# Kernel tuning notes

Hardware: AMD Instinct MI355X
Metric: run time of the kernel (lower is better)

## Reference

```python
import jax, jax.numpy as jnp
import numpy as np

KHS = 3        # kernel_half_size
SIGMA = 1.6    # sigma / dx
DX = 1.0
C = 20.0       # accumulate() hard-codes c = 20


def _gauss_kernel():
    size = 2 * KHS + 1
    g = np.arange(size, dtype=np.float32) - (size - 1) / 2.0
    g = np.exp(-(g / SIGMA) ** 2 / 2.0) / (SIGMA * np.sqrt(2.0 * np.pi))
    k = g[:, None, None] * g[None, :, None] * g[None, None, :]
    k = k / k.sum()
    return jnp.asarray(k[None, None], dtype=jnp.float32)  # [1,1,7,7,7]


def _smooth(x, kernel):
    # depthwise (single-channel) 3d gaussian conv, 'same' padding, zero bias
    return jax.lax.conv_general_dilated(
        x, kernel, window_strides=(1, 1, 1),
        padding=[(KHS, KHS)] * 3,
        dimension_numbers=("NCDHW", "OIDHW", "NCDHW"))


def _fdiff(f, axis):
    # forward difference, replicate last difference to keep size (torchJacobian3 style)
    d = jnp.diff(f, axis=axis)
    last = jax.lax.slice_in_dim(d, d.shape[axis] - 1, d.shape[axis], axis=axis)
    return jnp.concatenate([d, last], axis=axis)


def _curl(v):
    # v: [B,3,D,H,W]; per-channel fields are [B,D,H,W]; z->axis1, y->axis2, x->axis3
    u, vv, w = v[:, 0], v[:, 1], v[:, 2]
    cu = _fdiff(w, 2) - _fdiff(vv, 1)   # dw/dy - dv/dz
    cv = _fdiff(u, 1) - _fdiff(w, 3)    # du/dz - dw/dx
    cw = _fdiff(vv, 3) - _fdiff(u, 2)   # dv/dx - du/dy
    return jnp.stack([cu, cv, cw], axis=1)


def _integrate(t, v):
    # trapezoidal transmittance-weighted integral along depth (dim 2)
    front = (1.0 - t[:, :, 0]) * v[:, :, 0]
    trap = jnp.sum((t[:, :, :-1] - t[:, :, 1:]) * (v[:, :, :-1] + v[:, :, 1:]) * 0.5, axis=2)
    return front + trap


def setup_inputs() -> dict:
    key = jax.random.key(0)
    k1, k2 = jax.random.split(key)
    d = jax.random.uniform(k1, (4, 1, 128, 128, 128), dtype=jnp.float32)
    v = jax.random.normal(k2, (4, 3, 128, 128, 128), dtype=jnp.float32)
    return {"d": d, "v": v}


def reference(d, v):
    kern = _gauss_kernel()
    ds = _smooth(d, kern)
    vort = _curl(v) / DX
    vn = jnp.sqrt(jnp.sum(vort ** 2, axis=1, keepdims=True))  # [B,1,D,H,W]
    vn = _smooth(vn, kern)
    # single default view dir 'zp' -> identity rotation
    df = jnp.flip(ds, axis=2)
    vf = jnp.flip(vn, axis=2)
    x = jnp.cumsum(df * DX, axis=2)
    t = (x * C + 1.0) * jnp.exp(-C * x)
    iv = _integrate(t, vf)              # [B,1,H,W]
    return jnp.clip(iv, 0.0, 1.0)
```

## Files before the change

kernel.cpp:

```cpp
#include <hip/hip_runtime.h>
#include <math.h>

#define NB 4
#define DD 128
#define HH 128
#define WW 128
#define VOX (DD*HH*WW)
#define NVOX (NB*VOX)

struct GaussW { float w[7]; };
struct CurlIn { float4 wc, wyn, vc, vzn, uc, uzn, uyn; float wxp, vxp; };

__device__ __forceinline__ float4 f4zero() { float4 z; z.x = z.y = z.z = z.w = 0.f; return z; }

__device__ __forceinline__ CurlIn curl4_load(const float* __restrict__ u,
                                             const float* __restrict__ vv,
                                             const float* __restrict__ w,
                                             int z, int y, int x0) {
    int xq = x0 >> 2;
    size_t s = ((size_t)z << 14) | ((size_t)y << 7) | (size_t)x0;
    int dy = (y < 127) ? 128 : -128;
    int dz = (z < 127) ? 16384 : -16384;
    int dxp = (xq < 31) ? 4 : 0;
    CurlIn ci;
    ci.wc  = *(const float4*)(w  + s);
    ci.wyn = *(const float4*)(w  + s + dy);
    ci.vc  = *(const float4*)(vv + s);
    ci.vzn = *(const float4*)(vv + s + dz);
    ci.uc  = *(const float4*)(u  + s);
    ci.uzn = *(const float4*)(u  + s + dz);
    ci.uyn = *(const float4*)(u  + s + dy);
    ci.wxp = w [s + 3 + dxp];
    ci.vxp = vv[s + 3 + dxp];
    return ci;
}

__device__ __forceinline__ float4 curl4_math(const CurlIn& ci, int z, int y, int x0) {
    float sy = (y < 127) ? 1.f : -1.f;
    float sz = (z < 127) ? 1.f : -1.f;
    float wca[4] = {ci.wc.x, ci.wc.y, ci.wc.z, ci.wc.w};
    float vca[4] = {ci.vc.x, ci.vc.y, ci.vc.z, ci.vc.w};
    float wya[4] = {ci.wyn.x, ci.wyn.y, ci.wyn.z, ci.wyn.w};
    float vza[4] = {ci.vzn.x, ci.vzn.y, ci.vzn.z, ci.vzn.w};
    float uca[4] = {ci.uc.x, ci.uc.y, ci.uc.z, ci.uc.w};
    float uza[4] = {ci.uzn.x, ci.uzn.y, ci.uzn.z, ci.uzn.w};
    float uya[4] = {ci.uyn.x, ci.uyn.y, ci.uyn.z, ci.uyn.w};
    float wsh[4] = {ci.wc.y, ci.wc.z, ci.wc.w, ci.wxp};
    float vsh[4] = {ci.vc.y, ci.vc.z, ci.vc.w, ci.vxp};

    float4 o;
    float* oa = &o.x;
#pragma unroll
    for (int j = 0; j < 4; ++j) {
        int x = x0 + j;
        float fdxw = (x < 127) ? (wsh[j] - wca[j]) : (wca[3] - wca[2]);
        float fdxv = (x < 127) ? (vsh[j] - vca[j]) : (vca[3] - vca[2]);
        float fdyw = sy * (wya[j] - wca[j]);
        float fdyu = sy * (uya[j] - uca[j]);
        float fdzv = sz * (vza[j] - vca[j]);
        float fdzu = sz * (uza[j] - uca[j]);
        float cu = fdyw - fdzv;
        float cv = fdzu - fdxw;
        float cw = fdxv - fdyu;
        oa[j] = sqrtf(cu * cu + cv * cv + cw * cw);
    }
    return o;
}

__global__ __launch_bounds__(512, 2)
void yx_curl_dual_kernel(const float* __restrict__ dIn, float* __restrict__ P,
                         const float* __restrict__ v,   float* __restrict__ Q,
                         GaussW gw) {
    __shared__ float in_t[38][128];

    const int NT = 512;
    int bb = blockIdx.x;
    bool isCurl = (bb >= 2048);
    int b  = bb & 2047;
    int yq = b & 3;
    int z  = (b >> 2) & 127;
    int n  = b >> 9;
    int y0 = yq * 32;
    size_t slice = (((size_t)n << 7) | (size_t)z) << 14;
    int tid = threadIdx.x;

    if (!isCurl) {
        float4 Ld[3];
#pragma unroll
        for (int t = 0; t < 3; ++t) {
            int j  = tid + t * NT;
            int r  = j >> 5;
            int c4 = (j & 31) << 2;
            int gy = y0 - 3 + r;
            Ld[t] = (j < 1216 && gy >= 0 && gy < 128)
                  ? *(const float4*)(dIn + slice + ((size_t)gy << 7) + c4)
                  : f4zero();
        }
#pragma unroll
        for (int t = 0; t < 3; ++t) {
            int j = tid + t * NT;
            if (j < 1216) *(float4*)&in_t[j >> 5][(j & 31) << 2] = Ld[t];
        }
    } else {
        const float* u  = v + (size_t)n * 3 * VOX;
        const float* vv = u + VOX;
        const float* w  = vv + VOX;
        CurlIn ci[3];
        bool inb[3];
#pragma unroll
        for (int t = 0; t < 3; ++t) {
            int j  = tid + t * NT;
            int r  = j >> 5;
            int c4 = (j & 31) << 2;
            int gy = y0 - 3 + r;
            inb[t] = (j < 1216 && gy >= 0 && gy < 128);
            if (inb[t]) ci[t] = curl4_load(u, vv, w, z, gy, c4);
        }
#pragma unroll
        for (int t = 0; t < 3; ++t) {
            int j  = tid + t * NT;
            if (j < 1216) {
                int r  = j >> 5;
                int c4 = (j & 31) << 2;
                int gy = y0 - 3 + r;
                float4 val = inb[t] ? curl4_math(ci[t], z, gy, c4) : f4zero();
                *(float4*)&in_t[r][c4] = val;
            }
        }
    }
    __syncthreads();

    float4 rr[2];
#pragma unroll
    for (int t = 0; t < 2; ++t) {
        int j  = tid + t * NT;
        int yo = j >> 5;
        int c4 = (j & 31) << 2;
        float4 a = f4zero();
#pragma unroll
        for (int k = 0; k < 7; ++k) {
            float wk = gw.w[k];
            float4 tv = *(const float4*)&in_t[yo + k][c4];
            a.x += wk * tv.x; a.y += wk * tv.y; a.z += wk * tv.z; a.w += wk * tv.w;
        }
        rr[t] = a;
    }
    __syncthreads();

#pragma unroll
    for (int t = 0; t < 2; ++t) {
        int j  = tid + t * NT;
        *(float4*)&in_t[j >> 5][(j & 31) << 2] = rr[t];
    }
    __syncthreads();

    float* out = isCurl ? Q : P;
#pragma unroll
    for (int t = 0; t < 2; ++t) {
        int j   = tid + t * NT;
        int yo  = j >> 5;
        int x0c = (j & 31) << 2;
        float4 q0 = (x0c > 0)   ? *(const float4*)&in_t[yo][x0c - 4] : f4zero();
        float4 q1 =               *(const float4*)&in_t[yo][x0c];
        float4 q2 = (x0c < 124) ? *(const float4*)&in_t[yo][x0c + 4] : f4zero();
        float wdw[11] = {q0.y, q0.z, q0.w,
                         q1.x, q1.y, q1.z, q1.w,
                         q2.x, q2.y, q2.z, q2.w};
        float o[4];
#pragma unroll
        for (int j2 = 0; j2 < 4; ++j2) {
            float acc = 0.f;
#pragma unroll
            for (int k = 0; k < 7; ++k) acc += gw.w[k] * wdw[j2 + k];
            o[j2] = acc;
        }
        *(float4*)(out + slice + ((size_t)(y0 + yo) << 7) + x0c) =
            make_float4(o[0], o[1], o[2], o[3]);
    }
}

__global__ __launch_bounds__(256, 2)
void render_lds_kernel(const float* __restrict__ P, const float* __restrict__ Q,
                       float* __restrict__ out, GaussW gw) {
    __shared__ float Pl[128][64];
    __shared__ float Ql[128][64];
    __shared__ float csum[4][64];
    __shared__ float part[4][64];

    int tid = threadIdx.x;
    int bid = blockIdx.x;
    int col0 = bid << 6;
    int n  = col0 >> 14;
    int y  = (col0 >> 7) & 127;
    int x0 = col0 & 64;
    size_t base = ((size_t)n << 21) | ((size_t)y << 7) | (size_t)x0;

    int zrow = tid >> 4;
    int xq   = (tid & 15) << 2;
#pragma unroll
    for (int r = 0; r < 8; ++r) {
        int zi = (r << 4) + zrow;
        size_t off = base + ((size_t)zi << 14) + xq;
        *(float4*)&Pl[zi][xq] = *(const float4*)(P + off);
        *(float4*)&Ql[zi][xq] = *(const float4*)(Q + off);
    }
    __syncthreads();

    int xl = tid & 63;
    int ch = tid >> 6;
    int j0 = ch * 32;

    float a[38];
#pragma unroll
    for (int t = 0; t < 38; ++t) {
        int j = j0 - 3 + t;
        a[t] = (j >= 0 && j <= 127) ? Pl[127 - j][xl] : 0.f;
    }
#pragma unroll
    for (int i = 0; i < 32; ++i) {
        float s = 0.f;
#pragma unroll
        for (int k = 0; k < 7; ++k) s += gw.w[k] * a[i + k];
        a[i] = s;
    }
    float S = 0.f;
#pragma unroll
    for (int i = 0; i < 32; ++i) S += a[i];
    csum[ch][xl] = S;
    __syncthreads();

    float offset = 0.f;
    if (ch > 0) offset += csum[0][xl];
    if (ch > 1) offset += csum[1][xl];
    if (ch > 2) offset += csum[2][xl];

    float tp = 0.f, vp = 0.f, acc = 0.f, xacc = offset;
    if (ch > 0) {
        float v0 = 0.f;
#pragma unroll
        for (int k = 0; k < 7; ++k) {
            int j = j0 - 4 + k;
            v0 += gw.w[k] * Ql[127 - j][xl];
        }
        vp = v0;
        float xc = 20.f * offset;
        tp = (xc + 1.f) * __expf(-xc);
    }
#pragma unroll
    for (int i = 0; i < 32; ++i) {
        xacc += a[i];
        float vk = 0.f;
#pragma unroll
        for (int k = 0; k < 7; ++k) {
            int j = j0 + i - 3 + k;
            float qv = (j >= 0 && j <= 127) ? Ql[127 - j][xl] : 0.f;
            vk += gw.w[k] * qv;
        }
        float xc = 20.f * xacc;
        float tk = (xc + 1.f) * __expf(-xc);
        if (ch == 0 && i == 0) acc = (1.f - tk) * vk;
        else                   acc += (tp - tk) * (vp + vk) * 0.5f;
        tp = tk; vp = vk;
    }
    part[ch][xl] = acc;
    __syncthreads();

    if (ch == 0) {
        float r = part[0][xl] + part[1][xl] + part[2][xl] + part[3][xl];
        out[col0 + xl] = fminf(fmaxf(r, 0.f), 1.f);
    }
}

extern "C" void kernel_launch(void* const* d_in, const int* in_sizes, int n_in,
                              void* d_out, int out_size, void* d_ws, size_t ws_size,
                              hipStream_t stream) {
    const float* d = (const float*)d_in[0];
    const float* v = (const float*)d_in[1];
    float* out = (float*)d_out;

    GaussW gw;
    {
        double g[7], s = 0.0;
        for (int i = 0; i < 7; ++i) {
            double t = (i - 3) / 1.6;
            g[i] = exp(-t * t / 2.0);
            s += g[i];
        }
        for (int i = 0; i < 7; ++i) gw.w[i] = (float)(g[i] / s);
    }

    float* ws0 = (float*)d_ws;
    float* ws1 = ws0 + NVOX;

    yx_curl_dual_kernel<<<2 * NB * DD * 4, 512, 0, stream>>>(d, ws0, v, ws1, gw);

    render_lds_kernel<<<(NB * HH * WW) / 64, 256, 0, stream>>>(ws0, ws1, out, gw);
}
```

Before: 198.0 us.

## Split render depth into 8 chunks and reuse one LDS buffer for P and Q

The render kernel now runs 512 threads per block, and each column is split into 8 depth chunks of 16 instead of 4 chunks of 32. This halves the per-thread register arrays and loop length. A single 32KB LDS buffer is reused: P is loaded and smoothed first, then Q is loaded into the same buffer after a barrier, halving shared memory per block. This should raise occupancy and parallelism, at the cost of an extra serialized load phase, an extra barrier, and more halo overlap per chunk.

Measured after the change: 195.7 us. Within noise of the previous version (-1.2%).

```diff
diff --git a/kernel.cpp b/kernel.cpp
--- a/kernel.cpp
+++ b/kernel.cpp
@@ -179,13 +179,12 @@
     }
 }
 
-__global__ __launch_bounds__(256, 2)
-void render_lds_kernel(const float* __restrict__ P, const float* __restrict__ Q,
-                       float* __restrict__ out, GaussW gw) {
-    __shared__ float Pl[128][64];
-    __shared__ float Ql[128][64];
-    __shared__ float csum[4][64];
-    __shared__ float part[4][64];
+__global__ __launch_bounds__(512, 2)
+void render_z8_kernel(const float* __restrict__ P, const float* __restrict__ Q,
+                      float* __restrict__ out, GaussW gw) {
+    __shared__ float Buf[128][64];
+    __shared__ float csum[8][64];
+    __shared__ float part[8][64];
 
     int tid = threadIdx.x;
     int bid = blockIdx.x;
@@ -197,27 +196,26 @@
 
     int zrow = tid >> 4;
     int xq   = (tid & 15) << 2;
-#pragma unroll
-    for (int r = 0; r < 8; ++r) {
-        int zi = (r << 4) + zrow;
-        size_t off = base + ((size_t)zi << 14) + xq;
-        *(float4*)&Pl[zi][xq] = *(const float4*)(P + off);
-        *(float4*)&Ql[zi][xq] = *(const float4*)(Q + off);
+
+#pragma unroll
+    for (int r = 0; r < 4; ++r) {
+        int zi = (r << 5) + zrow;
+        *(float4*)&Buf[zi][xq] = *(const float4*)(P + base + ((size_t)zi << 14) + xq);
     }
     __syncthreads();
 
     int xl = tid & 63;
     int ch = tid >> 6;
-    int j0 = ch * 32;
-
-    float a[38];
-#pragma unroll
-    for (int t = 0; t < 38; ++t) {
+    int j0 = ch << 4;
+
+    float a[22];
+#pragma unroll
+    for (int t = 0; t < 22; ++t) {
         int j = j0 - 3 + t;
-        a[t] = (j >= 0 && j <= 127) ? Pl[127 - j][xl] : 0.f;
-    }
-#pragma unroll
-    for (int i = 0; i < 32; ++i) {
+        a[t] = (j >= 0 && j <= 127) ? Buf[127 - j][xl] : 0.f;
+    }
+#pragma unroll
+    for (int i = 0; i < 16; ++i) {
         float s = 0.f;
 #pragma unroll
         for (int k = 0; k < 7; ++k) s += gw.w[k] * a[i + k];
@@ -225,14 +223,19 @@
     }
     float S = 0.f;
 #pragma unroll
-    for (int i = 0; i < 32; ++i) S += a[i];
+    for (int i = 0; i < 16; ++i) S += a[i];
     csum[ch][xl] = S;
     __syncthreads();
 
+#pragma unroll
+    for (int r = 0; r < 4; ++r) {
+        int zi = (r << 5) + zrow;
+        *(float4*)&Buf[zi][xq] = *(const float4*)(Q + base + ((size_t)zi << 14) + xq);
+    }
     float offset = 0.f;
-    if (ch > 0) offset += csum[0][xl];
-    if (ch > 1) offset += csum[1][xl];
-    if (ch > 2) offset += csum[2][xl];
+#pragma unroll
+    for (int c = 0; c < 7; ++c) if (ch > c) offset += csum[c][xl];
+    __syncthreads();
 
     float tp = 0.f, vp = 0.f, acc = 0.f, xacc = offset;
     if (ch > 0) {
@@ -240,20 +243,20 @@
 #pragma unroll
         for (int k = 0; k < 7; ++k) {
             int j = j0 - 4 + k;
-            v0 += gw.w[k] * Ql[127 - j][xl];
+            v0 += gw.w[k] * Buf[127 - j][xl];
         }
         vp = v0;
         float xc = 20.f * offset;
         tp = (xc + 1.f) * __expf(-xc);
     }
 #pragma unroll
-    for (int i = 0; i < 32; ++i) {
+    for (int i = 0; i < 16; ++i) {
         xacc += a[i];
         float vk = 0.f;
 #pragma unroll
         for (int k = 0; k < 7; ++k) {
             int j = j0 + i - 3 + k;
-            float qv = (j >= 0 && j <= 127) ? Ql[127 - j][xl] : 0.f;
+            float qv = (j >= 0 && j <= 127) ? Buf[127 - j][xl] : 0.f;
             vk += gw.w[k] * qv;
         }
         float xc = 20.f * xacc;
@@ -266,7 +269,8 @@
     __syncthreads();
 
     if (ch == 0) {
-        float r = part[0][xl] + part[1][xl] + part[2][xl] + part[3][xl];
+        float r = part[0][xl] + part[1][xl] + part[2][xl] + part[3][xl]
+                + part[4][xl] + part[5][xl] + part[6][xl] + part[7][xl];
         out[col0 + xl] = fminf(fmaxf(r, 0.f), 1.f);
     }
 }
@@ -294,5 +298,5 @@
 
     yx_curl_dual_kernel<<<2 * NB * DD * 4, 512, 0, stream>>>(d, ws0, v, ws1, gw);
 
-    render_lds_kernel<<<(NB * HH * WW) / 64, 256, 0, stream>>>(ws0, ws1, out, gw);
-}
+    render_z8_kernel<<<(NB * HH * WW) / 64, 512, 0, stream>>>(ws0, ws1, out, gw);
+}
```
